# Performance work log

Hardware: AMD Instinct MI355X
Metric: run time of the kernel (lower is better)

Reference implementation:

```python
import jax, jax.numpy as jnp
import numpy as np

B_, S_, DM, DI, N_, R_, K_ = 2, 2048, 256, 512, 16, 32, 4
NB = 4  # 2 forward + 2 backward MambaBlocks


def setup_inputs() -> dict:
    key = jax.random.key(0)
    ks = jax.random.split(key, 16)
    def rn(k, shape, s=0.02):
        return jax.random.normal(k, shape, jnp.float32) * s
    A = jnp.log(jnp.arange(1, N_ + 1, dtype=jnp.float32))  # [N]
    return {
        'x': jax.random.normal(ks[0], (B_, S_, DM), jnp.float32),
        'in_w': rn(ks[1], (NB, DM, 2 * DI)),
        'conv_w': rn(ks[2], (NB, DI, K_), 0.3),
        'conv_b': jnp.zeros((NB, DI), jnp.float32),
        'A_log': jnp.broadcast_to(A, (NB, DI, N_)) + 0.0,
        'xd_w': rn(ks[3], (NB, DI, R_)),
        'xB_w': rn(ks[4], (NB, DI, N_)),
        'xC_w': rn(ks[5], (NB, DI, N_)),
        'dtp_w': rn(ks[6], (NB, R_, DI), R_ ** -0.5),
        'dtp_b': jax.random.uniform(ks[7], (NB, DI), jnp.float32,
                                    minval=jnp.log(0.001), maxval=jnp.log(0.1)),
        'D': jnp.ones((NB, DI), jnp.float32),
        'out_w': rn(ks[8], (NB, DI, DM)),
        'ln_g': jnp.ones((NB, DM), jnp.float32),
        'ln_b': jnp.zeros((NB, DM), jnp.float32),
        'merge_w': rn(ks[9], (2 * DM, DM)),
    }


def _layer_norm(x, g, b, eps=1e-5):
    m = jnp.mean(x, axis=-1, keepdims=True)
    v = jnp.mean(jnp.square(x - m), axis=-1, keepdims=True)
    return (x - m) * jax.lax.rsqrt(v + eps) * g + b


def _ssm_scan(dA, dBx, C):
    # dA, dBx: [B,S,DI,N]; C: [B,S,N] -> y: [B,S,DI]
    def step(h, inp):
        dA_t, dBx_t, C_t = inp
        h = dA_t * h + dBx_t                      # [B,DI,N]
        y = jnp.einsum('bdn,bn->bd', h, C_t)      # [B,DI]
        return h, y
    h0 = jnp.zeros(dA.shape[:1] + dA.shape[2:], dA.dtype)
    _, ys = jax.lax.scan(step, h0, (dA.transpose(1, 0, 2, 3),
                                    dBx.transpose(1, 0, 2, 3),
                                    C.transpose(1, 0, 2)))
    return ys.transpose(1, 0, 2)


def _mamba_block(x, in_w, conv_w, conv_b, A_log, xd_w, xB_w, xC_w,
                 dtp_w, dtp_b, D, out_w, g, b):
    res = x
    xn = _layer_norm(x, g, b)
    xz = xn @ in_w                                # [B,S,2*DI]
    xs, z = jnp.split(xz, 2, axis=-1)
    # causal depthwise conv: left pad K-1 (equals torch pad=K-1 then slice [:S])
    xc = jax.lax.conv_general_dilated(
        xs.transpose(0, 2, 1), conv_w[:, None, :], (1,), [(K_ - 1, 0)],
        dimension_numbers=('NCH', 'OIH', 'NCH'), feature_group_count=DI)
    xc = jax.nn.silu((xc + conv_b[None, :, None]).transpose(0, 2, 1))  # [B,S,DI]
    delta = jax.nn.softplus((xc @ xd_w) @ dtp_w + dtp_b)               # [B,S,DI]
    Bm = xc @ xB_w                                # [B,S,N]
    Cm = xc @ xC_w                                # [B,S,N]
    A = -jnp.exp(A_log)                           # [DI,N]
    dA = jnp.exp(delta[..., None] * A)            # [B,S,DI,N]
    dBx = (delta * xc)[..., None] * Bm[:, :, None, :]
    y = _ssm_scan(dA, dBx, Cm) + D * xc
    return (y * jax.nn.silu(z)) @ out_w + res


def reference(x, in_w, conv_w, conv_b, A_log, xd_w, xB_w, xC_w,
              dtp_w, dtp_b, D, out_w, ln_g, ln_b, merge_w):
    def blk(h, i):
        return _mamba_block(h, in_w[i], conv_w[i], conv_b[i], A_log[i],
                            xd_w[i], xB_w[i], xC_w[i], dtp_w[i], dtp_b[i],
                            D[i], out_w[i], ln_g[i], ln_b[i])
    fwd = blk(blk(x, 0), 1)
    bwd = blk(blk(x[:, ::-1], 2), 3)[:, ::-1]
    return jnp.concatenate([fwd, bwd], axis=-1) @ merge_w
```

## Files before the change

### kernel.cpp

```cpp
#include <hip/hip_runtime.h>

#define S_LEN 2048
#define DINNER 512
#define NCHUNK 64
#define CLEN 32

typedef unsigned short u16;
typedef short bf16x8 __attribute__((ext_vector_type(8)));
typedef unsigned short u16x8 __attribute__((ext_vector_type(8)));
typedef float f32x4 __attribute__((ext_vector_type(4)));

__device__ __forceinline__ float bf2f(u16 u) {
  unsigned int x = ((unsigned int)u) << 16;
  float f; __builtin_memcpy(&f, &x, 4); return f;
}
__device__ __forceinline__ u16 f2bf(float f) {
  unsigned int x; __builtin_memcpy(&x, &f, 4);
  return (u16)((x + 0x7FFFu + ((x >> 16) & 1u)) >> 16);
}
__device__ __forceinline__ float ldw(const void* p, size_t i, int isbf) {
  return isbf ? bf2f(((const u16*)p)[i]) : ((const float*)p)[i];
}
__device__ __forceinline__ float siluf(float x) { return x / (1.f + __expf(-x)); }
__device__ __forceinline__ float softplusf(float x) {
  if (x > 20.f) return x;
  return log1pf(__expf(x));
}

typedef __attribute__((address_space(1))) const void gvoid_t;
typedef __attribute__((address_space(3))) void lvoid_t;
__device__ __forceinline__ void glds16(const u16* g, u16* l) {
  __builtin_amdgcn_global_load_lds((gvoid_t*)g, (lvoid_t*)l, 16, 0, 0);
}

__global__ __launch_bounds__(256) void detect_kernel(const void* __restrict__ x,
                                                     int* __restrict__ flag) {
  __shared__ int cnt;
  if (threadIdx.x == 0) cnt = 0;
  __syncthreads();
  u16 u = ((const u16*)x)[2 * threadIdx.x];
  int e = (u >> 7) & 0xFF;
  if (e >= 0x60 && e <= 0x8F) atomicAdd(&cnt, 1);
  __syncthreads();
  if (threadIdx.x == 0) *flag = (cnt > 128) ? 1 : 0;
}

__global__ __launch_bounds__(256) void apack_kernel(
    const void* __restrict__ A_log, const int* __restrict__ pf, float* __restrict__ Acp)
{
  const int isbf = *pf;
  int idx = blockIdx.x * 256 + threadIdx.x;
  Acp[idx] = -__expf(ldw(A_log, (size_t)idx, isbf));
}

__global__ __launch_bounds__(256) void wpack_kernel(
    const void* __restrict__ src, const int* __restrict__ pf,
    u16* __restrict__ dst, int K, int N)
{
  const int isbf = *pf;
  __shared__ float tile[32][65];
  int nb64 = blockIdx.x, kb = blockIdx.y, mat = blockIdx.z;
  size_t so = (size_t)mat * K * N;
  int tid = threadIdx.x;
  int kk = tid >> 3, nseg = (tid & 7) * 8;
#pragma unroll
  for (int j = 0; j < 8; ++j)
    tile[kk][nseg + j] = ldw(src, so + (size_t)(kb * 32 + kk) * N + nb64 * 64 + nseg + j, isbf);
  __syncthreads();
  int cc = tid >> 6, i0 = (tid & 63) * 8;
  int q = i0 >> 7, nn = (i0 >> 3) & 15;
  u16 outv[8];
#pragma unroll
  for (int j = 0; j < 8; ++j) outv[j] = f2bf(tile[q * 8 + j][cc * 16 + nn]);
  size_t doff = (size_t)mat * K * N + ((size_t)(nb64 * 4 + cc) * (K >> 5) + kb) * 512 + i0;
  *(u16x8*)(dst + doff) = *(const u16x8*)outv;
}

__global__ __launch_bounds__(256) void wpack_cmb_kernel(
    const void* __restrict__ xdw, const void* __restrict__ dtpw,
    const void* __restrict__ xBw, const void* __restrict__ xCw,
    const int* __restrict__ pf, u16* __restrict__ dst)
{
  const int isbf = *pf;
  __shared__ float tile[32][65];
  int nb64 = blockIdx.x, kb = blockIdx.y, mat = blockIdx.z;
  int tid = threadIdx.x;
  if (nb64 < 8) {
    __shared__ float xd[32][33];
    __shared__ float wt[32][65];
    {
      int k = tid >> 3, j0 = (tid & 7) * 4;
#pragma unroll
      for (int j = 0; j < 4; ++j)
        xd[k][j0 + j] = ldw(xdw, (size_t)mat * 16384 + (size_t)(kb * 32 + k) * 32 + j0 + j, isbf);
      int jj = tid >> 3, n0l = (tid & 7) * 8;
#pragma unroll
      for (int n = 0; n < 8; ++n)
        wt[jj][n0l + n] = ldw(dtpw, (size_t)mat * 16384 + (size_t)jj * 512 + nb64 * 64 + n0l + n, isbf);
    }
    __syncthreads();
    for (int l = tid; l < 2048; l += 256) {
      int k = l >> 6, n = l & 63;
      float a = 0.f;
#pragma unroll
      for (int j = 0; j < 32; ++j) a += xd[k][j] * wt[j][n];
      tile[k][n] = a;
    }
  } else {
    for (int l = tid; l < 2048; l += 256) {
      int k = l >> 6, n = l & 63;
      int kg = kb * 32 + k;
      float v = 0.f;
      if (n < 16)      v = ldw(xBw, (size_t)mat * 8192 + (size_t)kg * 16 + n, isbf);
      else if (n < 32) v = ldw(xCw, (size_t)mat * 8192 + (size_t)kg * 16 + (n - 16), isbf);
      tile[k][n] = v;
    }
  }
  __syncthreads();
  int cc = tid >> 6, i0 = (tid & 63) * 8;
  int q = i0 >> 7, nn = (i0 >> 3) & 15;
  u16 outv[8];
#pragma unroll
  for (int j = 0; j < 8; ++j) outv[j] = f2bf(tile[q * 8 + j][cc * 16 + nn]);
  size_t doff = (size_t)mat * 294912 + ((size_t)(nb64 * 4 + cc) * 16 + kb) * 512 + i0;
  *(u16x8*)(dst + doff) = *(const u16x8*)outv;
}

__global__ __launch_bounds__(256) void ln_kernel(
    const void* __restrict__ x, const u16* __restrict__ obA, int it,
    const void* __restrict__ g, const void* __restrict__ bta,
    const int* __restrict__ pf, float* __restrict__ res, u16* __restrict__ xnb)
{
  const int isbf = *pf;
  int r = blockIdx.x;
  int tid = threadIdx.x;
  int chain = r >> 12, rr = r & 4095;
  int i = chain * 2 + it;
  size_t wo = (size_t)i * 256;
  float v;
  if (it == 0) {
    int b = rr >> 11, s = rr & 2047;
    int sr = chain ? (b * S_LEN + (S_LEN - 1 - s)) : rr;
    v = ldw(x, (size_t)sr * 256 + tid, isbf);
  } else {
    v = bf2f(obA[(size_t)r * 256 + tid]);
  }
  res[(size_t)r * 256 + tid] = v;
  float s1 = v, s2 = v * v;
#pragma unroll
  for (int o = 32; o > 0; o >>= 1) {
    s1 += __shfl_xor(s1, o, 64);
    s2 += __shfl_xor(s2, o, 64);
  }
  __shared__ float r1[4], r2[4];
  if ((tid & 63) == 0) { r1[tid >> 6] = s1; r2[tid >> 6] = s2; }
  __syncthreads();
  s1 = r1[0] + r1[1] + r1[2] + r1[3];
  s2 = r2[0] + r2[1] + r2[2] + r2[3];
  float mean = s1 * (1.f / 256.f);
  float var  = s2 * (1.f / 256.f) - mean * mean;
  float inv  = rsqrtf(var + 1e-5f);
  xnb[(size_t)r * 256 + tid] =
      f2bf((v - mean) * inv * ldw(g, wo + tid, isbf) + ldw(bta, wo + tid, isbf));
}

template<int OUTMODE>
__global__ __launch_bounds__(256) void gemm64(
    const u16* __restrict__ A, const u16* __restrict__ Wp, size_t woA, size_t woB, int mhalf,
    const float* __restrict__ res, void* __restrict__ Out, void* __restrict__ Out2,
    const void* __restrict__ bias, size_t boA, size_t boB,
    const int* __restrict__ pf, int N, int K, int nbx)
{
  const int isbf = *pf;
  __shared__ __align__(16) u16 Asb[2 * 64 * 32];
  __shared__ __align__(16) u16 Bsb[2 * 64 * 32];
  int tid = threadIdx.x;
  int gidx = blockIdx.x;
  int xcd = gidx & 7, rest = gidx >> 3;
  int nIdx = rest % nbx, mGrp = rest / nbx;
  int n0 = nIdx * 64, m0 = (xcd + (mGrp << 3)) * 64;
  size_t wo = (mhalf && m0 >= mhalf) ? woB : woA;
  int w = tid >> 6, lane = tid & 63;
  int q = lane >> 4, r = lane & 15;
  const int wm0 = (w >> 1) * 2, wn0 = (w & 1) * 2;
  const int kbs = K >> 5;
  f32x4 acc[2][2];
#pragma unroll
  for (int i = 0; i < 2; ++i)
#pragma unroll
    for (int j = 0; j < 2; ++j) acc[i][j] = (f32x4){0.f, 0.f, 0.f, 0.f};

  const u16* asrc = A + (size_t)(m0 + (w << 4) + (lane & 15)) * K + ((lane >> 4) << 3);
  u16* albase = Asb + w * 512;
  const size_t bbase = wo + (size_t)((n0 >> 4) + w) * kbs * 512 + lane * 8;
  u16* blbase = Bsb + w * 512;

  for (int k0 = 0; k0 < K; k0 += 64) {
    glds16(asrc + k0,        albase);
    glds16(asrc + k0 + 32,   albase + 2048);
    const u16* bsrc = Wp + bbase + (size_t)(k0 >> 5) * 512;
    glds16(bsrc,       blbase);
    glds16(bsrc + 512, blbase + 2048);
    __syncthreads();
#pragma unroll
    for (int ck = 0; ck < 2; ++ck) {
      const u16* Ab = Asb + ck * 2048;
      const u16* Bb = Bsb + ck * 2048;
      bf16x8 af[2], bfr[2];
#pragma unroll
      for (int i = 0; i < 2; ++i)
        af[i] = *(const bf16x8*)(Ab + ((wm0 + i) * 4 + q) * 128 + r * 8);
#pragma unroll
      for (int j = 0; j < 2; ++j)
        bfr[j] = *(const bf16x8*)(Bb + ((wn0 + j) * 4 + q) * 128 + r * 8);
#pragma unroll
      for (int i = 0; i < 2; ++i)
#pragma unroll
        for (int j = 0; j < 2; ++j)
          acc[i][j] = __builtin_amdgcn_mfma_f32_16x16x32_bf16(af[i], bfr[j], acc[i][j], 0, 0, 0);
    }
    __syncthreads();
  }
#pragma unroll
  for (int i = 0; i < 2; ++i) {
    int rowb = m0 + (wm0 + i) * 16 + q * 4;
#pragma unroll
    for (int j = 0; j < 2; ++j) {
      int col = n0 + (wn0 + j) * 16 + r;
#pragma unroll
      for (int t = 0; t < 4; ++t) {
        int row = rowb + t;
        float v = acc[i][j][t];
        if (OUTMODE == 2 || OUTMODE == 3) { if (res) v += res[(size_t)row * N + col]; }
        if (OUTMODE == 1) {
          size_t lidx = (size_t)row * N + col;
          if (isbf) ((u16*)Out)[lidx] = f2bf(v); else ((float*)Out)[lidx] = v;
        } else if (OUTMODE == 2) {
          ((u16*)Out)[(size_t)row * N + col] = f2bf(v);
        } else if (OUTMODE == 3) {
          int orow, cofx;
          if (row < 4096) { orow = row; cofx = 0; }
          else {
            int rr = row - 4096; int bb = rr >> 11, ss = rr & 2047;
            orow = bb * S_LEN + (S_LEN - 1 - ss); cofx = 256;
          }
          ((u16*)Out)[(size_t)orow * 512 + col + cofx] = f2bf(v);
        } else if (OUTMODE == 5) {
          if (col < 512) {
            float bv = ldw(bias, ((row < 4096) ? boA : boB) + col, isbf);
            ((u16*)Out)[(size_t)row * 512 + col] = f2bf(softplusf(v + bv));
          } else if (col < 544) {
            ((float*)Out2)[(size_t)row * 32 + (col - 512)] = v;
          }
        }
      }
    }
  }
}

__global__ __launch_bounds__(256) void conv_kernel(
    const u16* __restrict__ xzb, const void* __restrict__ cw, const void* __restrict__ cb,
    int it, const int* __restrict__ pf, u16* __restrict__ xcb)
{
  const int isbf = *pf;
  int idx = blockIdx.x * 256 + threadIdx.x;
  int r = idx >> 6, dg = idx & 63;
  int d0 = dg << 3;
  int chain = r >> 12, rr = r & 4095;
  int i = chain * 2 + it;
  size_t ow = (size_t)i * 2048, ob = (size_t)i * 512;
  int s = rr & 2047;
  float acc[8];
#pragma unroll
  for (int j = 0; j < 8; ++j) acc[j] = ldw(cb, ob + d0 + j, isbf);
#pragma unroll
  for (int k = 0; k < 4; ++k) {
    int t = s - 3 + k;
    if (t >= 0) {
      u16x8 xv = *(const u16x8*)(xzb + (((size_t)(r + t - s)) << 10) + d0);
#pragma unroll
      for (int j = 0; j < 8; ++j)
        acc[j] += ldw(cw, ow + (size_t)(d0 + j) * 4 + k, isbf) * bf2f(xv[j]);
    }
  }
  u16 outv[8];
#pragma unroll
  for (int j = 0; j < 8; ++j) outv[j] = f2bf(siluf(acc[j]));
  *(u16x8*)(xcb + ((size_t)r << 9) + d0) = *(const u16x8*)outv;
}

__global__ __launch_bounds__(256) void scan_p1_kernel(
    const u16* __restrict__ xcb, const u16* __restrict__ delb, const float* __restrict__ dBC,
    const float* __restrict__ Acp, int it, const int* __restrict__ pf,
    float* __restrict__ aggA, float* __restrict__ aggB)
{
  __shared__ float sb[32][16];
  __shared__ u16 sdu[32][64];
  __shared__ u16 sxu[32][64];
  int tid = threadIdx.x;
  int di = tid >> 2, ng = tid & 3;
  int d0 = blockIdx.x << 6;
  int c = blockIdx.y, seq = blockIdx.z;
  int chain = seq >> 1, bb = seq & 1;
  int row0 = chain * 4096 + bb * S_LEN + c * CLEN;
  int i = chain * 2 + it;
  {
    int t = tid >> 3, e0 = (tid & 7) * 8;
    *(u16x8*)&sdu[t][e0] = *(const u16x8*)(delb + (size_t)(row0 + t) * 512 + d0 + e0);
    *(u16x8*)&sxu[t][e0] = *(const u16x8*)(xcb + (size_t)(row0 + t) * 512 + d0 + e0);
  }
  if (tid < 128) {
    int t = tid >> 2, e0 = (tid & 3) * 4;
    *(f32x4*)&sb[t][e0] = *(const f32x4*)(dBC + (size_t)(row0 + t) * 32 + e0);
  }
  f32x4 Ac = *(const f32x4*)(Acp + ((size_t)i * 512 + d0 + di) * 16 + ng * 4);
  __syncthreads();
  float h[4] = {0.f, 0.f, 0.f, 0.f};
  float ap[4] = {1.f, 1.f, 1.f, 1.f};
#pragma unroll 8
  for (int t = 0; t < CLEN; ++t) {
    float de = bf2f(sdu[t][di]);
    float dx = de * bf2f(sxu[t][di]);
    f32x4 B = *(const f32x4*)&sb[t][ng * 4];
#pragma unroll
    for (int j = 0; j < 4; ++j) {
      float e = __expf(de * Ac[j]);
      h[j] = e * h[j] + dx * B[j];
      ap[j] *= e;
    }
  }
  size_t o = (((size_t)(seq * NCHUNK + c) * DINNER) + d0 + di) * 16 + ng * 4;
  *(f32x4*)(aggA + o) = (f32x4){ap[0], ap[1], ap[2], ap[3]};
  *(f32x4*)(aggB + o) = (f32x4){h[0], h[1], h[2], h[3]};
}

__global__ __launch_bounds__(64) void scan_prefix_kernel(
    const float* __restrict__ aggA, float* __restrict__ aggB)
{
  int idx = blockIdx.x * 64 + threadIdx.x;
  int n = idx & 15, d = (idx >> 4) & 511, seq = idx >> 13;
  size_t o = (((size_t)(seq * NCHUNK) * DINNER) + d) * 16 + n;
  float a = aggA[o], t = aggB[o];
  float h = 0.f;
  for (int c = 0; c < NCHUNK; ++c) {
    size_t on = o + (size_t)DINNER * 16;
    float an = 0.f, tn = 0.f;
    if (c + 1 < NCHUNK) { an = aggA[on]; tn = aggB[on]; }
    aggB[o] = h;
    h = a * h + t;
    a = an; t = tn;
    o = on;
  }
}

__global__ __launch_bounds__(256) void scan_p3_kernel(
    const u16* __restrict__ xcb, const u16* __restrict__ delb, const float* __restrict__ dBC,
    const u16* __restrict__ xzb, const float* __restrict__ hpref,
    const float* __restrict__ Acp, const void* __restrict__ Dp,
    int it, const int* __restrict__ pf, u16* __restrict__ ymb)
{
  const int isbf = *pf;
  __shared__ float sbc[32][32];
  __shared__ float sy[32][64];
  __shared__ u16 sdu[32][64];
  __shared__ u16 sxu[32][64];
  __shared__ u16 szu[32][64];
  int tid = threadIdx.x;
  int di = tid >> 2, ng = tid & 3;
  int d0 = blockIdx.x << 6;
  int c = blockIdx.y, seq = blockIdx.z;
  int chain = seq >> 1, bb = seq & 1;
  int row0 = chain * 4096 + bb * S_LEN + c * CLEN;
  int i = chain * 2 + it;
  size_t oD = (size_t)i * 512;
  {
    int t = tid >> 3, e0 = (tid & 7) * 8;
    *(u16x8*)&sdu[t][e0] = *(const u16x8*)(delb + (size_t)(row0 + t) * 512 + d0 + e0);
    *(u16x8*)&sxu[t][e0] = *(const u16x8*)(xcb + (size_t)(row0 + t) * 512 + d0 + e0);
    *(u16x8*)&szu[t][e0] = *(const u16x8*)(xzb + ((size_t)(row0 + t) << 10) + 512 + d0 + e0);
  }
  {
    int t = tid >> 3, e0 = (tid & 7) * 4;
    *(f32x4*)&sbc[t][e0] = *(const f32x4*)(dBC + (size_t)(row0 + t) * 32 + e0);
  }
  f32x4 Ac = *(const f32x4*)(Acp + ((size_t)i * 512 + d0 + di) * 16 + ng * 4);
  float Dv = ldw(Dp, oD + d0 + di, isbf);
  float h[4];
  size_t o = (((size_t)(seq * NCHUNK + c) * DINNER) + d0 + di) * 16 + ng * 4;
  {
    f32x4 v = *(const f32x4*)(hpref + o);
    h[0] = v[0]; h[1] = v[1]; h[2] = v[2]; h[3] = v[3];
  }
  __syncthreads();
#pragma unroll 8
  for (int t = 0; t < CLEN; ++t) {
    float de = bf2f(sdu[t][di]);
    float xv = bf2f(sxu[t][di]);
    float dx = de * xv;
    f32x4 B = *(const f32x4*)&sbc[t][ng * 4];
    f32x4 C = *(const f32x4*)&sbc[t][16 + ng * 4];
    float yc = 0.f;
#pragma unroll
    for (int j = 0; j < 4; ++j) {
      float e = __expf(de * Ac[j]);
      h[j] = e * h[j] + dx * B[j];
      yc += h[j] * C[j];
    }
    yc += __shfl_xor(yc, 1, 64);
    yc += __shfl_xor(yc, 2, 64);
    if (ng == 0) sy[t][di] = yc + Dv * xv;
  }
  __syncthreads();
  int dcol = tid & 63;
#pragma unroll
  for (int k = 0; k < 8; ++k) {
    int t = (tid >> 6) + k * 4;
    float y = sy[t][dcol];
    float z = bf2f(szu[t][dcol]);
    ymb[(size_t)(row0 + t) * 512 + d0 + dcol] = f2bf(y * siluf(z));
  }
}

extern "C" void kernel_launch(void* const* d_in, const int* in_sizes, int n_in,
                              void* d_out, int out_size, void* d_ws, size_t ws_size,
                              hipStream_t stream)
{
  const void* x       = d_in[0];
  const void* in_w    = d_in[1];
  const void* conv_w  = d_in[2];
  const void* conv_b  = d_in[3];
  const void* A_log   = d_in[4];
  const void* xd_w    = d_in[5];
  const void* xB_w    = d_in[6];
  const void* xC_w    = d_in[7];
  const void* dtp_w   = d_in[8];
  const void* dtp_b   = d_in[9];
  const void* Dp      = d_in[10];
  const void* out_w   = d_in[11];
  const void* ln_g    = d_in[12];
  const void* ln_b    = d_in[13];
  const void* merge_w = d_in[14];

  float* ws    = (float*)d_ws;
  float* res   = ws;
  float* dBC   = res + (size_t)8192 * 256;
  float* aggA  = dBC + (size_t)8192 * 32;
  float* aggB  = aggA + (size_t)2097152;
  u16*   xz_bf = (u16*)(aggB + (size_t)2097152);
  u16*   xc_bf = xz_bf + (size_t)8192 * 1024;
  u16*   del_bf= xc_bf + (size_t)8192 * 512;
  u16*   Wp_in = del_bf + (size_t)8192 * 512;
  u16*   Wp_out= Wp_in + (size_t)4 * 262144;
  u16*   Wp_mg = Wp_out + (size_t)4 * 131072;
  u16*   Wp_cmb= Wp_mg + (size_t)131072;
  float* Acp   = (float*)(Wp_cmb + (size_t)4 * 294912);
  int*   flagp = (int*)(Acp + (size_t)4 * 8192);
  u16*   obA_bf= xz_bf;
  u16*   xn_bf = (u16*)aggA;
  u16*   ym_bf = (u16*)aggA;
  u16*   cat_bf= del_bf;

  dim3 blk(256);
  hipLaunchKernelGGL(detect_kernel, dim3(1), blk, 0, stream, x, flagp);
  hipLaunchKernelGGL(apack_kernel, dim3(128), blk, 0, stream, A_log, flagp, Acp);
  hipLaunchKernelGGL(wpack_kernel, dim3(16, 8, 4), blk, 0, stream, in_w, flagp, Wp_in, 256, 1024);
  hipLaunchKernelGGL(wpack_kernel, dim3(4, 16, 4), blk, 0, stream, out_w, flagp, Wp_out, 512, 256);
  hipLaunchKernelGGL(wpack_kernel, dim3(4, 16, 1), blk, 0, stream, merge_w, flagp, Wp_mg, 512, 256);
  hipLaunchKernelGGL(wpack_cmb_kernel, dim3(9, 16, 4), blk, 0, stream,
      xd_w, dtp_w, xB_w, xC_w, flagp, Wp_cmb);

  for (int it = 0; it < 2; ++it) {
    hipLaunchKernelGGL(ln_kernel, dim3(8192), blk, 0, stream,
        x, obA_bf, it, ln_g, ln_b, flagp, res, xn_bf);
    hipLaunchKernelGGL((gemm64<2>), dim3(16 * 128), blk, 0, stream,
        xn_bf, Wp_in, (size_t)it * 262144, (size_t)(2 + it) * 262144, 4096,
        (const float*)nullptr, (void*)xz_bf, (void*)nullptr,
        (const void*)nullptr, (size_t)0, (size_t)0, flagp, 1024, 256, 16);
    hipLaunchKernelGGL(conv_kernel, dim3(2048), blk, 0, stream,
        xz_bf, conv_w, conv_b, it, flagp, xc_bf);
    hipLaunchKernelGGL((gemm64<5>), dim3(9 * 128), blk, 0, stream,
        xc_bf, Wp_cmb, (size_t)it * 294912, (size_t)(2 + it) * 294912, 4096,
        (const float*)nullptr, (void*)del_bf, (void*)dBC,
        dtp_b, (size_t)it * 512, (size_t)(2 + it) * 512, flagp, 576, 512, 9);
    hipLaunchKernelGGL(scan_p1_kernel, dim3(8, NCHUNK, 4), blk, 0, stream,
        xc_bf, del_bf, dBC, Acp, it, flagp, aggA, aggB);
    hipLaunchKernelGGL(scan_prefix_kernel, dim3(512), dim3(64), 0, stream, aggA, aggB);
    hipLaunchKernelGGL(scan_p3_kernel, dim3(8, NCHUNK, 4), blk, 0, stream,
        xc_bf, del_bf, dBC, xz_bf, aggB, Acp, Dp, it, flagp, ym_bf);
    if (it == 0) {
      hipLaunchKernelGGL((gemm64<2>), dim3(4 * 128), blk, 0, stream,
          ym_bf, Wp_out, (size_t)0, (size_t)2 * 131072, 4096,
          res, (void*)obA_bf, (void*)nullptr,
          (const void*)nullptr, (size_t)0, (size_t)0, flagp, 256, 512, 4);
    } else {
      hipLaunchKernelGGL((gemm64<3>), dim3(4 * 128), blk, 0, stream,
          ym_bf, Wp_out, (size_t)1 * 131072, (size_t)3 * 131072, 4096,
          res, (void*)cat_bf, (void*)nullptr,
          (const void*)nullptr, (size_t)0, (size_t)0, flagp, 256, 512, 4);
    }
  }
  hipLaunchKernelGGL((gemm64<1>), dim3(4 * 64), blk, 0, stream,
      cat_bf, Wp_mg, (size_t)0, (size_t)0, 0,
      (const float*)nullptr, d_out, (void*)nullptr,
      (const void*)nullptr, (size_t)0, (size_t)0, flagp, 256, 512, 4);
}
```

Before: 432.0 us.

## Fuse weight-packing kernels into one prep launch and drop LDS-direct loads in GEMM

Merges the A-pack, three weight-pack and combined-weight-pack kernels into a single prep kernel dispatched on block index. This removes four launches and their serial gaps. Separately, the GEMM tile loader stops using global_load_lds DMA and instead does ordinary vector loads into registers followed by LDS stores, with a new thread-to-tile mapping. That trades the direct-to-LDS path for register staging, which may cost extra VGPRs and instructions per tile.

```diff
diff --git a/kernel.cpp b/kernel.cpp
--- a/kernel.cpp
+++ b/kernel.cpp
@@ -25,12 +25,6 @@
 __device__ __forceinline__ float softplusf(float x) {
   if (x > 20.f) return x;
   return log1pf(__expf(x));
-}
-
-typedef __attribute__((address_space(1))) const void gvoid_t;
-typedef __attribute__((address_space(3))) void lvoid_t;
-__device__ __forceinline__ void glds16(const u16* g, u16* l) {
-  __builtin_amdgcn_global_load_lds((gvoid_t*)g, (lvoid_t*)l, 16, 0, 0);
 }
 
 __global__ __launch_bounds__(256) void detect_kernel(const void* __restrict__ x,
@@ -45,85 +39,99 @@
   if (threadIdx.x == 0) *flag = (cnt > 128) ? 1 : 0;
 }
 
-__global__ __launch_bounds__(256) void apack_kernel(
-    const void* __restrict__ A_log, const int* __restrict__ pf, float* __restrict__ Acp)
-{
-  const int isbf = *pf;
-  int idx = blockIdx.x * 256 + threadIdx.x;
-  Acp[idx] = -__expf(ldw(A_log, (size_t)idx, isbf));
-}
-
-__global__ __launch_bounds__(256) void wpack_kernel(
-    const void* __restrict__ src, const int* __restrict__ pf,
-    u16* __restrict__ dst, int K, int N)
-{
-  const int isbf = *pf;
-  __shared__ float tile[32][65];
-  int nb64 = blockIdx.x, kb = blockIdx.y, mat = blockIdx.z;
-  size_t so = (size_t)mat * K * N;
-  int tid = threadIdx.x;
-  int kk = tid >> 3, nseg = (tid & 7) * 8;
-#pragma unroll
-  for (int j = 0; j < 8; ++j)
-    tile[kk][nseg + j] = ldw(src, so + (size_t)(kb * 32 + kk) * N + nb64 * 64 + nseg + j, isbf);
-  __syncthreads();
-  int cc = tid >> 6, i0 = (tid & 63) * 8;
-  int q = i0 >> 7, nn = (i0 >> 3) & 15;
-  u16 outv[8];
-#pragma unroll
-  for (int j = 0; j < 8; ++j) outv[j] = f2bf(tile[q * 8 + j][cc * 16 + nn]);
-  size_t doff = (size_t)mat * K * N + ((size_t)(nb64 * 4 + cc) * (K >> 5) + kb) * 512 + i0;
-  *(u16x8*)(dst + doff) = *(const u16x8*)outv;
-}
-
-__global__ __launch_bounds__(256) void wpack_cmb_kernel(
+__global__ __launch_bounds__(256) void prep_kernel(
+    const void* __restrict__ A_log,
+    const void* __restrict__ in_w, const void* __restrict__ out_w,
+    const void* __restrict__ merge_w,
     const void* __restrict__ xdw, const void* __restrict__ dtpw,
     const void* __restrict__ xBw, const void* __restrict__ xCw,
-    const int* __restrict__ pf, u16* __restrict__ dst)
+    const int* __restrict__ pf,
+    float* __restrict__ Acp, u16* __restrict__ Wp_in, u16* __restrict__ Wp_out,
+    u16* __restrict__ Wp_mg, u16* __restrict__ Wp_cmb)
 {
   const int isbf = *pf;
-  __shared__ float tile[32][65];
-  int nb64 = blockIdx.x, kb = blockIdx.y, mat = blockIdx.z;
+  int b = blockIdx.x;
   int tid = threadIdx.x;
-  if (nb64 < 8) {
-    __shared__ float xd[32][33];
-    __shared__ float wt[32][65];
-    {
-      int k = tid >> 3, j0 = (tid & 7) * 4;
-#pragma unroll
-      for (int j = 0; j < 4; ++j)
-        xd[k][j0 + j] = ldw(xdw, (size_t)mat * 16384 + (size_t)(kb * 32 + k) * 32 + j0 + j, isbf);
-      int jj = tid >> 3, n0l = (tid & 7) * 8;
-#pragma unroll
-      for (int n = 0; n < 8; ++n)
-        wt[jj][n0l + n] = ldw(dtpw, (size_t)mat * 16384 + (size_t)jj * 512 + nb64 * 64 + n0l + n, isbf);
-    }
+  __shared__ float smem[32 * 163];
+  float* tile = smem;
+
+  if (b < 128) {
+    int idx = b * 256 + tid;
+    Acp[idx] = -__expf(ldw(A_log, (size_t)idx, isbf));
+    return;
+  }
+  b -= 128;
+
+  if (b < 512 + 256 + 64) {
+    const void* src; u16* dst; int K, N, nb64, kb, mat;
+    if (b < 512)      { src = in_w;    dst = Wp_in;  K = 256; N = 1024;
+                        nb64 = b % 16; kb = (b / 16) % 8; mat = b / 128; }
+    else if (b < 768) { int c = b - 512; src = out_w; dst = Wp_out; K = 512; N = 256;
+                        nb64 = c % 4; kb = (c / 4) % 16; mat = c / 64; }
+    else              { int c = b - 768; src = merge_w; dst = Wp_mg; K = 512; N = 256;
+                        nb64 = c % 4; kb = (c / 4) % 16; mat = 0; }
+    size_t so = (size_t)mat * K * N;
+    int kk = tid >> 3, nseg = (tid & 7) * 8;
+#pragma unroll
+    for (int j = 0; j < 8; ++j)
+      tile[kk * 65 + nseg + j] =
+          ldw(src, so + (size_t)(kb * 32 + kk) * N + nb64 * 64 + nseg + j, isbf);
     __syncthreads();
-    for (int l = tid; l < 2048; l += 256) {
-      int k = l >> 6, n = l & 63;
-      float a = 0.f;
-#pragma unroll
-      for (int j = 0; j < 32; ++j) a += xd[k][j] * wt[j][n];
-      tile[k][n] = a;
-    }
-  } else {
-    for (int l = tid; l < 2048; l += 256) {
-      int k = l >> 6, n = l & 63;
-      int kg = kb * 32 + k;
-      float v = 0.f;
-      if (n < 16)      v = ldw(xBw, (size_t)mat * 8192 + (size_t)kg * 16 + n, isbf);
-      else if (n < 32) v = ldw(xCw, (size_t)mat * 8192 + (size_t)kg * 16 + (n - 16), isbf);
-      tile[k][n] = v;
-    }
-  }
-  __syncthreads();
-  int cc = tid >> 6, i0 = (tid & 63) * 8;
-  int q = i0 >> 7, nn = (i0 >> 3) & 15;
-  u16 outv[8];
-#pragma unroll
-  for (int j = 0; j < 8; ++j) outv[j] = f2bf(tile[q * 8 + j][cc * 16 + nn]);
-  size_t doff = (size_t)mat * 294912 + ((size_t)(nb64 * 4 + cc) * 16 + kb) * 512 + i0;
-  *(u16x8*)(dst + doff) = *(const u16x8*)outv;
+    int cc = tid >> 6, i0 = (tid & 63) * 8;
+    int q = i0 >> 7, nn = (i0 >> 3) & 15;
+    u16 outv[8];
+#pragma unroll
+    for (int j = 0; j < 8; ++j) outv[j] = f2bf(tile[(q * 8 + j) * 65 + cc * 16 + nn]);
+    size_t doff = (size_t)mat * K * N + ((size_t)(nb64 * 4 + cc) * (K >> 5) + kb) * 512 + i0;
+    *(u16x8*)(dst + doff) = *(const u16x8*)outv;
+    return;
+  }
+  b -= 832;
+
+  {
+    int nb64 = b % 9, kb = (b / 9) % 16, mat = b / 144;
+    float* xd = smem + 32 * 65;
+    float* wt = smem + 32 * 98;
+    if (nb64 < 8) {
+      {
+        int k = tid >> 3, j0 = (tid & 7) * 4;
+#pragma unroll
+        for (int j = 0; j < 4; ++j)
+          xd[k * 33 + j0 + j] =
+              ldw(xdw, (size_t)mat * 16384 + (size_t)(kb * 32 + k) * 32 + j0 + j, isbf);
+        int jj = tid >> 3, n0l = (tid & 7) * 8;
+#pragma unroll
+        for (int n = 0; n < 8; ++n)
+          wt[jj * 65 + n0l + n] =
+              ldw(dtpw, (size_t)mat * 16384 + (size_t)jj * 512 + nb64 * 64 + n0l + n, isbf);
+      }
+      __syncthreads();
+      for (int l = tid; l < 2048; l += 256) {
+        int k = l >> 6, n = l & 63;
+        float a = 0.f;
+#pragma unroll
+        for (int j = 0; j < 32; ++j) a += xd[k * 33 + j] * wt[j * 65 + n];
+        tile[k * 65 + n] = a;
+      }
+    } else {
+      for (int l = tid; l < 2048; l += 256) {
+        int k = l >> 6, n = l & 63;
+        int kg = kb * 32 + k;
+        float v = 0.f;
+        if (n < 16)      v = ldw(xBw, (size_t)mat * 8192 + (size_t)kg * 16 + n, isbf);
+        else if (n < 32) v = ldw(xCw, (size_t)mat * 8192 + (size_t)kg * 16 + (n - 16), isbf);
+        tile[k * 65 + n] = v;
+      }
+    }
+    __syncthreads();
+    int cc = tid >> 6, i0 = (tid & 63) * 8;
+    int q = i0 >> 7, nn = (i0 >> 3) & 15;
+    u16 outv[8];
+#pragma unroll
+    for (int j = 0; j < 8; ++j) outv[j] = f2bf(tile[(q * 8 + j) * 65 + cc * 16 + nn]);
+    size_t doff = (size_t)mat * 294912 + ((size_t)(nb64 * 4 + cc) * 16 + kb) * 512 + i0;
+    *(u16x8*)(Wp_cmb + doff) = *(const u16x8*)outv;
+  }
 }
 
 __global__ __launch_bounds__(256) void ln_kernel(
@@ -190,17 +198,18 @@
 #pragma unroll
     for (int j = 0; j < 2; ++j) acc[i][j] = (f32x4){0.f, 0.f, 0.f, 0.f};
 
-  const u16* asrc = A + (size_t)(m0 + (w << 4) + (lane & 15)) * K + ((lane >> 4) << 3);
-  u16* albase = Asb + w * 512;
-  const size_t bbase = wo + (size_t)((n0 >> 4) + w) * kbs * 512 + lane * 8;
-  u16* blbase = Bsb + w * 512;
+  int sm = tid >> 2, sq = tid & 3;
+  const u16* asrc = A + (size_t)(m0 + sm) * K + sq * 8;
+  u16* adst = Asb + ((sm >> 4) * 4 + sq) * 128 + (sm & 15) * 8;
+  int bnb = tid >> 6, binner = (tid & 63) * 8;
+  u16* bdst = Bsb + bnb * 512 + binner;
 
   for (int k0 = 0; k0 < K; k0 += 64) {
-    glds16(asrc + k0,        albase);
-    glds16(asrc + k0 + 32,   albase + 2048);
-    const u16* bsrc = Wp + bbase + (size_t)(k0 >> 5) * 512;
-    glds16(bsrc,       blbase);
-    glds16(bsrc + 512, blbase + 2048);
+    *(u16x8*)adst          = *(const u16x8*)(asrc + k0);
+    *(u16x8*)(adst + 2048) = *(const u16x8*)(asrc + k0 + 32);
+    const u16* bsrc = Wp + wo + ((size_t)((n0 >> 4) + bnb) * kbs + (k0 >> 5)) * 512 + binner;
+    *(u16x8*)bdst          = *(const u16x8*)bsrc;
+    *(u16x8*)(bdst + 2048) = *(const u16x8*)(bsrc + 512);
     __syncthreads();
 #pragma unroll
     for (int ck = 0; ck < 2; ++ck) {
@@ -462,12 +471,9 @@
 
   dim3 blk(256);
   hipLaunchKernelGGL(detect_kernel, dim3(1), blk, 0, stream, x, flagp);
-  hipLaunchKernelGGL(apack_kernel, dim3(128), blk, 0, stream, A_log, flagp, Acp);
-  hipLaunchKernelGGL(wpack_kernel, dim3(16, 8, 4), blk, 0, stream, in_w, flagp, Wp_in, 256, 1024);
-  hipLaunchKernelGGL(wpack_kernel, dim3(4, 16, 4), blk, 0, stream, out_w, flagp, Wp_out, 512, 256);
-  hipLaunchKernelGGL(wpack_kernel, dim3(4, 16, 1), blk, 0, stream, merge_w, flagp, Wp_mg, 512, 256);
-  hipLaunchKernelGGL(wpack_cmb_kernel, dim3(9, 16, 4), blk, 0, stream,
-      xd_w, dtp_w, xB_w, xC_w, flagp, Wp_cmb);
+  hipLaunchKernelGGL(prep_kernel, dim3(1536), blk, 0, stream,
+      A_log, in_w, out_w, merge_w, xd_w, dtp_w, xB_w, xC_w, flagp,
+      Acp, Wp_in, Wp_out, Wp_mg, Wp_cmb);
 
   for (int it = 0; it < 2; ++it) {
     hipLaunchKernelGGL(ln_kernel, dim3(8192), blk, 0, stream,
```

Measured after the change: 409.3 us. 1.06x faster.
